# Optimization experiments

Hardware: AMD Instinct MI355X
Metric: run time of the kernel (lower is better)

Reference implementation:

```python
import jax, jax.numpy as jnp
import numpy as np

L = 4            # n_layers
D_MODEL = 768
D_STATE = 16
D_CONV = 4
EXPAND = 2
D_INNER = EXPAND * D_MODEL      # 1536
DT_RANK = (D_MODEL + 15) // 16  # 48
B = 2
T = 2048
LN_EPS = 1e-5


def setup_inputs() -> dict:
    key = jax.random.key(0)
    ks = jax.random.split(key, 12)
    s = 0.02
    x = jax.random.normal(ks[0], (B, T, D_MODEL), dtype=jnp.float32)
    in_proj_w = jax.random.normal(ks[1], (L, 2 * D_INNER, D_MODEL), dtype=jnp.float32) * s
    conv_w = jax.random.normal(ks[2], (L, D_INNER, D_CONV), dtype=jnp.float32) * s
    conv_b = jnp.zeros((L, D_INNER), dtype=jnp.float32)
    x_proj_w = jax.random.normal(ks[3], (L, DT_RANK + 2 * D_STATE, D_INNER), dtype=jnp.float32) * s
    dt_proj_w = jax.random.normal(ks[4], (L, D_INNER, DT_RANK), dtype=jnp.float32) * s
    dt_proj_b = jax.random.normal(ks[5], (L, D_INNER), dtype=jnp.float32) * 0.1
    # Standard S4D-real init: A = -[1..d_state], stored as log
    A_log = jnp.log(jnp.broadcast_to(
        jnp.arange(1, D_STATE + 1, dtype=jnp.float32), (L, D_INNER, D_STATE)))
    D_param = jnp.ones((L, D_INNER), dtype=jnp.float32)
    out_proj_w = jax.random.normal(ks[6], (L, D_MODEL, D_INNER), dtype=jnp.float32) * s
    ln_g = jnp.ones((L, D_MODEL), dtype=jnp.float32)
    ln_b = jnp.zeros((L, D_MODEL), dtype=jnp.float32)
    return {"x": x, "in_proj_w": in_proj_w, "conv_w": conv_w, "conv_b": conv_b,
            "x_proj_w": x_proj_w, "dt_proj_w": dt_proj_w, "dt_proj_b": dt_proj_b,
            "A_log": A_log, "D_param": D_param, "out_proj_w": out_proj_w,
            "ln_g": ln_g, "ln_b": ln_b}


def _layernorm(x, g, b):
    mu = jnp.mean(x, axis=-1, keepdims=True)
    var = jnp.mean(jnp.square(x - mu), axis=-1, keepdims=True)
    return (x - mu) * jax.lax.rsqrt(var + LN_EPS) * g + b


def _mamba_layer(x, inw, convw, convb, xpw, dtw, dtb, A_log, Dp, outw):
    # x: [B,T,d_model]
    Tn = x.shape[1]
    xz = jnp.einsum('btd,ed->bte', x, inw)          # [B,T,2*d_inner]
    xin, z = jnp.split(xz, 2, axis=-1)              # each [B,T,d_inner]
    # causal depthwise conv1d over time (kernel d_conv)
    xp = jnp.pad(xin, ((0, 0), (D_CONV - 1, 0), (0, 0)))
    xc = convb
    for k in range(D_CONV):
        xc = xc + xp[:, k:k + Tn, :] * convw[:, k]
    xc = jax.nn.silu(xc)                            # [B,T,d_inner]
    dbl = jnp.einsum('bti,ei->bte', xc, xpw)        # [B,T,dt_rank+2*d_state]
    dt, Bs, Cs = jnp.split(dbl, [DT_RANK, DT_RANK + D_STATE], axis=-1)
    dt = jax.nn.softplus(jnp.einsum('btr,dr->btd', dt, dtw) + dtb)  # [B,T,d_inner]
    A = -jnp.exp(A_log)                             # [d_inner,d_state]
    dA = jnp.exp(jnp.einsum('btd,dn->btdn', dt, A))  # discretized A
    dBu = (dt * xc)[..., None] * Bs[:, :, None, :]   # [B,T,d_inner,d_state]

    def step(h, inp):
        dA_t, dBu_t, C_t = inp                      # [B,d,n],[B,d,n],[B,n]
        h = dA_t * h + dBu_t
        y = jnp.einsum('bdn,bn->bd', h, C_t)
        return h, y

    h0 = jnp.zeros((x.shape[0], D_INNER, D_STATE), x.dtype)
    _, ys = jax.lax.scan(step, h0,
                         (jnp.swapaxes(dA, 0, 1), jnp.swapaxes(dBu, 0, 1),
                          jnp.swapaxes(Cs, 0, 1)))
    y = jnp.swapaxes(ys, 0, 1) + xc * Dp            # skip connection D*u
    y = y * jax.nn.silu(z)                          # gate
    return jnp.einsum('bti,ei->bte', y, outw)       # [B,T,d_model]


def reference(x, in_proj_w, conv_w, conv_b, x_proj_w, dt_proj_w, dt_proj_b,
              A_log, D_param, out_proj_w, ln_g, ln_b):
    for l in range(L):
        residual = x
        h = _mamba_layer(x, in_proj_w[l], conv_w[l], conv_b[l], x_proj_w[l],
                         dt_proj_w[l], dt_proj_b[l], A_log[l], D_param[l],
                         out_proj_w[l])
        h = _layernorm(h, ln_g[l], ln_b[l])
        x = h + residual                            # dropout=0 -> identity
    return x
```

## Files before the change

kernel.cpp:

```cpp
#include <hip/hip_runtime.h>

#define T_LEN 2048
#define DM    768
#define DI    1536
#define DS    16
#define BB    2
#define NROWS (BB * T_LEN)
#define NCH   64
#define CLEN  32
#define NSEG  8
#define SEGC  8

#define OFF_DTB 0
#define OFF_A   6144
#define OFF_DP  104448
#define OFF_CW  110592
#define OFF_CB  135168
#define OFF_LG  141312
#define OFF_LB  144384
#define PRM_TOT 147456

typedef __attribute__((ext_vector_type(8))) short bh8;
typedef __attribute__((ext_vector_type(4))) float f32x4;

typedef const __attribute__((address_space(1))) void as1_void;
typedef __attribute__((address_space(3))) void as3_void;

__device__ __forceinline__ void glds16(const void* g, void* l) {
    __builtin_amdgcn_global_load_lds((as1_void*)g, (as3_void*)l, 16, 0, 0);
}

__device__ __forceinline__ float bf2f(unsigned short u) {
    return __uint_as_float(((unsigned)u) << 16);
}
__device__ __forceinline__ unsigned short f2bf(float f) {
    unsigned u = __float_as_uint(f);
    u += 0x7FFFu + ((u >> 16) & 1u);
    return (unsigned short)(u >> 16);
}

__device__ __forceinline__ void ld8(const void* p, long e0, int bf, float* v) {
    if (bf) {
        bh8 u = *(const bh8*)((const unsigned short*)p + e0);
#pragma unroll
        for (int j = 0; j < 8; ++j) v[j] = bf2f((unsigned short)u[j]);
    } else {
        const f32x4* q = (const f32x4*)((const float*)p + e0);
        f32x4 a = q[0], b = q[1];
#pragma unroll
        for (int j = 0; j < 4; ++j) { v[j] = a[j]; v[4 + j] = b[j]; }
    }
}

__device__ __forceinline__ void cp8(unsigned short* dst, long de0,
                                    const void* src, long se0, int bf) {
    if (bf) {
        *(bh8*)&dst[de0] = *(const bh8*)((const unsigned short*)src + se0);
    } else {
        const f32x4* q = (const f32x4*)((const float*)src + se0);
        f32x4 a = q[0], b = q[1];
        bh8 o;
#pragma unroll
        for (int j = 0; j < 4; ++j) { o[j] = (short)f2bf(a[j]); o[4 + j] = (short)f2bf(b[j]); }
        *(bh8*)&dst[de0] = o;
    }
}

__global__ void k_sniff(const unsigned short* __restrict__ x, int* __restrict__ flag) {
    __shared__ int cnt[4];
    int tid = threadIdx.x;
    int local = 0;
#pragma unroll
    for (int j = 0; j < 4; ++j) {
        unsigned short u = x[tid * 4 + j];
        int e = (u >> 7) & 0xFF;
        if (e >= 100 && e <= 140) local++;
    }
    for (int off = 32; off; off >>= 1) local += __shfl_down(local, off, 64);
    if ((tid & 63) == 0) cnt[tid >> 6] = local;
    __syncthreads();
    if (tid == 0) {
        int tot = cnt[0] + cnt[1] + cnt[2] + cnt[3];
        *flag = (tot >= 900) ? 1 : 0;
    }
}

__global__ void k_prep(const void* in_x, const void* in_inw, const void* in_ow,
                       const void* in_xpw, const void* in_dtw,
                       const void* dtb, const void* alog, const void* dpar,
                       const void* cw, const void* cb, const void* lg, const void* lb,
                       unsigned short* __restrict__ xbf, float* __restrict__ xf,
                       unsigned short* __restrict__ Win, unsigned short* __restrict__ Wout,
                       unsigned short* __restrict__ Wxp, unsigned short* __restrict__ Wdt,
                       float* __restrict__ prm, float* __restrict__ dblz,
                       const int* __restrict__ flag) {
    const long G0 = 393216L;
    const long G1 = G0 + 1179648L;
    const long G2 = G1 + 589824L;
    const long G3 = G2 + 98304L;
    const long G4 = G3 + 49152L;
    const long G5 = G4 + 18432L;
    const long G6 = G5 + 65536L;
    int bf = *flag;
    long g = (long)blockIdx.x * 256 + threadIdx.x;
    if (g >= G6) return;
    if (g < G0) {
        long e0 = g * 8;
        float v[8];
        ld8(in_x, e0, bf, v);
        bh8 o;
#pragma unroll
        for (int j = 0; j < 8; ++j) o[j] = (short)f2bf(v[j]);
        *(bh8*)&xbf[e0] = o;
        f32x4 a, b;
#pragma unroll
        for (int j = 0; j < 4; ++j) { a[j] = v[j]; b[j] = v[4 + j]; }
        ((f32x4*)&xf[e0])[0] = a;
        ((f32x4*)&xf[e0])[1] = b;
    } else if (g < G1) {
        long e0 = (g - G0) * 8;
        cp8(Win, e0, in_inw, e0, bf);
    } else if (g < G2) {
        long e0 = (g - G1) * 8;
        cp8(Wout, e0, in_ow, e0, bf);
    } else if (g < G3) {
        long e0 = (g - G2) * 8;
        int c = (int)(e0 % 1536);
        long rl = e0 / 1536;
        int r = (int)(rl % 128);
        int l = (int)(rl / 128);
        if (r < 80) cp8(Wxp, e0, in_xpw, ((long)l * 80 + r) * 1536 + c, bf);
        else        *(bh8*)&Wxp[e0] = (bh8)(short)0;
    } else if (g < G4) {
        long e0 = (g - G3) * 8;
        int c = (int)(e0 & 63);
        long rl = e0 >> 6;
        int d = (int)(rl % 1536);
        int l = (int)(rl / 1536);
        if (c < 48) cp8(Wdt, e0, in_dtw, ((long)l * 1536 + d) * 48 + c, bf);
        else        *(bh8*)&Wdt[e0] = (bh8)(short)0;
    } else if (g < G5) {
        long e0 = (g - G4) * 8;
        float v[8];
        if (e0 < OFF_A)        ld8(dtb,  e0 - OFF_DTB, bf, v);
        else if (e0 < OFF_DP) {
            ld8(alog, e0 - OFF_A, bf, v);
#pragma unroll
            for (int j = 0; j < 8; ++j) v[j] = -__expf(v[j]);
        }
        else if (e0 < OFF_CW)  ld8(dpar, e0 - OFF_DP, bf, v);
        else if (e0 < OFF_CB)  ld8(cw,   e0 - OFF_CW, bf, v);
        else if (e0 < OFF_LG)  ld8(cb,   e0 - OFF_CB, bf, v);
        else if (e0 < OFF_LB)  ld8(lg,   e0 - OFF_LG, bf, v);
        else                   ld8(lb,   e0 - OFF_LB, bf, v);
        f32x4 a, b;
#pragma unroll
        for (int j = 0; j < 4; ++j) { a[j] = v[j]; b[j] = v[4 + j]; }
        ((f32x4*)&prm[e0])[0] = a;
        ((f32x4*)&prm[e0])[1] = b;
    } else {
        long e0 = (g - G5) * 8;
        f32x4 z = {0.f, 0.f, 0.f, 0.f};
        ((f32x4*)&dblz[e0])[0] = z;
        ((f32x4*)&dblz[e0])[1] = z;
    }
}

__global__ __launch_bounds__(256) void k_gemm128(const unsigned short* __restrict__ A,
                                                 const unsigned short* __restrict__ B,
                                                 unsigned short* __restrict__ C,
                                                 int M, int N, int K) {
    __shared__ __align__(16) unsigned short As[128 * 32];
    __shared__ __align__(16) unsigned short Bs[128 * 32];
    const int tid = threadIdx.x;
    const int lane = tid & 63, wid = tid >> 6;
    const int wm = wid >> 1, wn = wid & 1;
    const int id = blockIdx.y * 24 + blockIdx.x;
    const int xcd = id & 7, loc = id >> 3;
    const int bx = (xcd & 1) * 12 + loc % 12;
    const int by = (xcd >> 1) * 8 + loc / 12;
    const long arow0 = (long)by * 128;
    const long bcol0 = (long)bx * 128;
    const int r16 = lane >> 2;
    const int c8  = (lane & 3) * 8;
    f32x4 acc[4][4] = {};

    for (int k0 = 0; k0 < K; k0 += 32) {
#pragma unroll
        for (int j = 0; j < 2; ++j) {
            int chunk = wid + j * 4;
            int row = chunk * 16 + r16;
            glds16(&A[(arow0 + row) * K + k0 + c8], &As[chunk * 512]);
            glds16(&B[(bcol0 + row) * K + k0 + c8], &Bs[chunk * 512]);
        }
        __syncthreads();
        const int row = lane & 15, q8 = (lane >> 4) * 8;
        bh8 af[4], bfr[4];
#pragma unroll
        for (int i = 0; i < 4; ++i) af[i] = *(const bh8*)&As[(wm * 64 + i * 16 + row) * 32 + q8];
#pragma unroll
        for (int i = 0; i < 4; ++i) bfr[i] = *(const bh8*)&Bs[(wn * 64 + i * 16 + row) * 32 + q8];
#pragma unroll
        for (int i = 0; i < 4; ++i)
#pragma unroll
            for (int j = 0; j < 4; ++j)
                acc[i][j] = __builtin_amdgcn_mfma_f32_16x16x32_bf16(af[i], bfr[j], acc[i][j], 0, 0, 0);
        __syncthreads();
    }
    const int crow = (lane >> 4) * 4, ccol = lane & 15;
#pragma unroll
    for (int i = 0; i < 4; ++i)
#pragma unroll
        for (int j = 0; j < 4; ++j)
#pragma unroll
            for (int r = 0; r < 4; ++r) {
                long gr = arow0 + wm * 64 + i * 16 + crow + r;
                long gc = bcol0 + wn * 64 + j * 16 + ccol;
                C[gr * N + gc] = f2bf(acc[i][j][r]);
            }
}

__global__ __launch_bounds__(256) void k_xproj(const unsigned short* __restrict__ xz,
                                               const unsigned short* __restrict__ B,
                                               const float* __restrict__ cw,
                                               const float* __restrict__ cb,
                                               float* __restrict__ C) {
    __shared__ __align__(16) unsigned short As[64 * 32];
    __shared__ __align__(16) unsigned short Bs[64 * 32];
    const int tid = threadIdx.x;
    const int lane = tid & 63, w = tid >> 6;
    const int wm = w >> 1, wn = w & 1;
    const long arow0 = (long)blockIdx.y * 64;
    const long bcol0 = (long)blockIdx.x * 64;
    const int kbase = blockIdx.z * 384;
    const int r4 = lane >> 2;
    const int c8 = (lane & 3) * 8;
    const int t_o = tid >> 2;
    const int dl  = (tid & 3) * 8;
    const int sp  = (int)((arow0 + t_o) & (T_LEN - 1));
    f32x4 acc[2][2] = {};

    for (int kk = 0; kk < 384; kk += 32) {
        const int k0 = kbase + kk;
        glds16(&B[(bcol0 + w * 16 + r4) * DI + k0 + c8], &Bs[w * 512]);
        const int dg = k0 + dl;
        float xv[4][8];
#pragma unroll
        for (int rr = 0; rr < 4; ++rr) {
            if (sp - 3 + rr >= 0) {
                bh8 u = *(const bh8*)&xz[(arow0 + t_o - 3 + rr) * 3072 + dg];
#pragma unroll
                for (int q = 0; q < 8; ++q) xv[rr][q] = bf2f((unsigned short)u[q]);
            } else {
#pragma unroll
                for (int q = 0; q < 8; ++q) xv[rr][q] = 0.f;
            }
        }
        bh8 o;
#pragma unroll
        for (int q = 0; q < 8; ++q) {
            const f32x4 w4 = *(const f32x4*)&cw[(dg + q) * 4];
            float a = cb[dg + q] + w4[0] * xv[0][q] + w4[1] * xv[1][q]
                                 + w4[2] * xv[2][q] + w4[3] * xv[3][q];
            a = a / (1.f + __expf(-a));
            o[q] = (short)f2bf(a);
        }
        *(bh8*)&As[t_o * 32 + dl] = o;
        __syncthreads();
        const int row2 = lane & 15, q8 = (lane >> 4) * 8;
        bh8 af[2], bfr[2];
#pragma unroll
        for (int i = 0; i < 2; ++i) af[i] = *(const bh8*)&As[(wm * 32 + i * 16 + row2) * 32 + q8];
#pragma unroll
        for (int i = 0; i < 2; ++i) bfr[i] = *(const bh8*)&Bs[(wn * 32 + i * 16 + row2) * 32 + q8];
#pragma unroll
        for (int i = 0; i < 2; ++i)
#pragma unroll
            for (int j = 0; j < 2; ++j)
                acc[i][j] = __builtin_amdgcn_mfma_f32_16x16x32_bf16(af[i], bfr[j], acc[i][j], 0, 0, 0);
        __syncthreads();
    }
    const int crow = (lane >> 4) * 4, ccol = lane & 15;
#pragma unroll
    for (int i = 0; i < 2; ++i)
#pragma unroll
        for (int j = 0; j < 2; ++j)
#pragma unroll
            for (int r = 0; r < 4; ++r) {
                long gr = arow0 + wm * 32 + i * 16 + crow + r;
                long gc = bcol0 + wn * 32 + j * 16 + ccol;
                atomicAdd(&C[gr * 128 + gc], acc[i][j][r]);
            }
}

__global__ __launch_bounds__(256) void k_dtproj(const float* __restrict__ Dbl,
                                                const unsigned short* __restrict__ Wdt,
                                                const float* __restrict__ bias,
                                                unsigned short* __restrict__ Dt) {
    __shared__ __align__(16) unsigned short As[2 * 64 * 32];
    __shared__ __align__(16) unsigned short Bs[2 * 64 * 32];
    const int tid = threadIdx.x;
    const int lane = tid & 63, wid = tid >> 6;
    const int wm = wid >> 1, wn = wid & 1;
    const long arow0 = (long)blockIdx.y * 64;
    const long bcol0 = (long)blockIdx.x * 64;

    {
        int r = tid >> 2;
        int cs = (tid & 3) * 16;
        unsigned short tmp[16];
#pragma unroll
        for (int q = 0; q < 4; ++q) {
            int col0 = cs + q * 4;
            if (col0 < 48) {
                f32x4 v = *(const f32x4*)&Dbl[(arow0 + r) * 128 + col0];
#pragma unroll
                for (int j = 0; j < 4; ++j) tmp[q * 4 + j] = f2bf(v[j]);
            } else {
#pragma unroll
                for (int j = 0; j < 4; ++j) tmp[q * 4 + j] = 0;
            }
        }
        int p = cs >> 5;
        int cp = cs & 31;
        *(bh8*)&As[p * 2048 + r * 32 + cp]     = *(bh8*)&tmp[0];
        *(bh8*)&As[p * 2048 + r * 32 + cp + 8] = *(bh8*)&tmp[8];
    }
#pragma unroll
    for (int j = 0; j < 2; ++j) {
        int chunk = tid + j * 256;
        int p = chunk >> 8;
        int rem = chunk & 255;
        int row = rem >> 2;
        int c4 = rem & 3;
        glds16(&Wdt[(bcol0 + row) * 64 + p * 32 + c4 * 8], &Bs[chunk * 8]);
    }
    __syncthreads();

    const int row2 = lane & 15, q8 = (lane >> 4) * 8;
    f32x4 acc[2][2] = {};
#pragma unroll
    for (int p = 0; p < 2; ++p) {
        bh8 af[2], bfr[2];
#pragma unroll
        for (int i = 0; i < 2; ++i) af[i] = *(const bh8*)&As[p * 2048 + (wm * 32 + i * 16 + row2) * 32 + q8];
#pragma unroll
        for (int i = 0; i < 2; ++i) bfr[i] = *(const bh8*)&Bs[p * 2048 + (wn * 32 + i * 16 + row2) * 32 + q8];
#pragma unroll
        for (int i = 0; i < 2; ++i)
#pragma unroll
            for (int j = 0; j < 2; ++j)
                acc[i][j] = __builtin_amdgcn_mfma_f32_16x16x32_bf16(af[i], bfr[j], acc[i][j], 0, 0, 0);
    }
    const int crow = (lane >> 4) * 4, ccol = lane & 15;
#pragma unroll
    for (int i = 0; i < 2; ++i)
#pragma unroll
        for (int j = 0; j < 2; ++j)
#pragma unroll
            for (int r = 0; r < 4; ++r) {
                long gr = arow0 + wm * 32 + i * 16 + crow + r;
                long gc = bcol0 + wn * 32 + j * 16 + ccol;
                float v = acc[i][j][r] + bias[gc];
                v = (v > 20.f) ? v : log1pf(__expf(v));
                Dt[gr * DI + gc] = f2bf(v);
            }
}

__global__ __launch_bounds__(256) void k_outproj(const unsigned short* __restrict__ A,
                                                 const unsigned short* __restrict__ B,
                                                 float* __restrict__ C) {
    __shared__ __align__(16) unsigned short As[64 * 32];
    __shared__ __align__(16) unsigned short Bs[64 * 32];
    const int tid = threadIdx.x;
    const int lane = tid & 63, wid = tid >> 6;
    const int wm = wid >> 1, wn = wid & 1;
    const int id = blockIdx.y * 12 + blockIdx.x;
    const int xcd = id & 7, loc = id >> 3;
    const int bx = (xcd & 1) * 6 + loc % 6;
    const int by = (xcd >> 1) * 16 + loc / 6;
    const long arow0 = (long)by * 64;
    const long bcol0 = (long)bx * 64;
    const int r16 = lane >> 2;
    const int c8  = (lane & 3) * 8;
    f32x4 acc[2][2] = {};

    for (int k0 = 0; k0 < DI; k0 += 32) {
        int row = wid * 16 + r16;
        glds16(&A[(arow0 + row) * DI + k0 + c8], &As[wid * 512]);
        glds16(&B[(bcol0 + row) * DI + k0 + c8], &Bs[wid * 512]);
        __syncthreads();
        const int row2 = lane & 15, q8 = (lane >> 4) * 8;
        bh8 af[2], bfr[2];
#pragma unroll
        for (int i = 0; i < 2; ++i) af[i] = *(const bh8*)&As[(wm * 32 + i * 16 + row2) * 32 + q8];
#pragma unroll
        for (int i = 0; i < 2; ++i) bfr[i] = *(const bh8*)&Bs[(wn * 32 + i * 16 + row2) * 32 + q8];
#pragma unroll
        for (int i = 0; i < 2; ++i)
#pragma unroll
            for (int j = 0; j < 2; ++j)
                acc[i][j] = __builtin_amdgcn_mfma_f32_16x16x32_bf16(af[i], bfr[j], acc[i][j], 0, 0, 0);
        __syncthreads();
    }
    const int crow = (lane >> 4) * 4, ccol = lane & 15;
#pragma unroll
    for (int i = 0; i < 2; ++i)
#pragma unroll
        for (int j = 0; j < 2; ++j)
#pragma unroll
            for (int r = 0; r < 4; ++r) {
                long gr = arow0 + wm * 32 + i * 16 + crow + r;
                long gc = bcol0 + wn * 32 + j * 16 + ccol;
                C[gr * DM + gc] = acc[i][j][r];
            }
}

__global__ __launch_bounds__(256) void k_scan1(const unsigned short* __restrict__ dt,
                                               const unsigned short* __restrict__ xz,
                                               const float* __restrict__ dbl,
                                               const float* __restrict__ An,
                                               const float* __restrict__ cw,
                                               const float* __restrict__ cb,
                                               float* __restrict__ hch,
                                               float* __restrict__ sdtb) {
    __shared__ __align__(16) float Bsh[CLEN * 16];
    const int tid = threadIdx.x;
    const int lane = tid & 63, w = tid >> 6;
    const int db = blockIdx.x % 6;
    const int c  = (blockIdx.x / 6) % NCH;
    const int b  = blockIdx.x / (6 * NCH);
    const int d  = db * 256 + tid;
    const int t0 = c * CLEN;
    const long rowb = (long)b * T_LEN + t0;
    if (w < 2) {
        int t = w * 16 + (lane >> 2);
        int nq = lane & 3;
        glds16(&dbl[(rowb + t) * 128 + 48 + nq * 4], &Bsh[w * 256]);
    }
    float h[DS], An_r[DS];
    const f32x4* Ap = (const f32x4*)(An + (long)d * DS);
#pragma unroll
    for (int q = 0; q < 4; ++q) {
        f32x4 a4 = Ap[q];
#pragma unroll
        for (int j = 0; j < 4; ++j) { An_r[q * 4 + j] = a4[j]; h[q * 4 + j] = 0.f; }
    }
    const f32x4 w4 = *(const f32x4*)&cw[d * 4];
    const float cbv = cb[d];
    float x1, x2, x3;
    if (c == 0) { x1 = x2 = x3 = 0.f; }
    else {
        x1 = bf2f(xz[(rowb - 1) * 3072 + d]);
        x2 = bf2f(xz[(rowb - 2) * 3072 + d]);
        x3 = bf2f(xz[(rowb - 3) * 3072 + d]);
    }
    __syncthreads();
    float sdt = 0.f;
#pragma unroll 4
    for (int s = 0; s < CLEN; ++s) {
        long bt = rowb + s;
        float xt = bf2f(xz[bt * 3072 + d]);
        float a = cbv + w4[0] * x3 + w4[1] * x2 + w4[2] * x1 + w4[3] * xt;
        float xcv = a / (1.f + __expf(-a));
        x3 = x2; x2 = x1; x1 = xt;
        float dtv = bf2f(dt[bt * DI + d]);
        const f32x4* bp = (const f32x4*)&Bsh[s * 16];
        float du = dtv * xcv;
        sdt += dtv;
#pragma unroll
        for (int q = 0; q < 4; ++q) {
            f32x4 b4 = bp[q];
#pragma unroll
            for (int j = 0; j < 4; ++j) {
                int n = q * 4 + j;
                h[n] = __expf(An_r[n] * dtv) * h[n] + du * b4[j];
            }
        }
    }
    long o = (((long)b * NCH + c) * DI + d) * DS;
    f32x4* hp = (f32x4*)(hch + o);
#pragma unroll
    for (int q = 0; q < 4; ++q) {
        f32x4 h4;
#pragma unroll
        for (int j = 0; j < 4; ++j) h4[j] = h[q * 4 + j];
        hp[q] = h4;
    }
    sdtb[((long)b * NCH + c) * DI + d] = sdt;
}

__global__ __launch_bounds__(256) void k_scan2a(float* __restrict__ hbuf,
                                                const float* __restrict__ sdtb,
                                                const float* __restrict__ An,
                                                float* __restrict__ cum,
                                                float* __restrict__ Gseg,
                                                float* __restrict__ Sseg) {
    long gid = (long)blockIdx.x * 256 + threadIdx.x;
    int n = (int)(gid & 15);
    long t = gid >> 4;
    int d  = (int)(t % DI);
    int sg = (int)((t / DI) & (NSEG - 1));
    int b  = (int)(t / (DI * NSEG));
    float an = An[(long)d * DS + n];
    float h = 0.f, cs = 0.f;
    for (int i = 0; i < SEGC; ++i) {
        int c = sg * SEGC + i;
        long rowi = ((long)b * NCH + c) * DI + d;
        long idx = rowi * DS + n;
        float sdt = sdtb[rowi];
        float g = hbuf[idx];
        hbuf[idx] = h;
        if (n == 0) cum[rowi] = cs;
        h = __expf(an * sdt) * h + g;
        cs += sdt;
    }
    long gi = (((long)b * NSEG + sg) * DI + d) * DS + n;
    Gseg[gi] = h;
    if (n == 0) Sseg[((long)b * NSEG + sg) * DI + d] = cs;
}

__global__ __launch_bounds__(256) void k_scan3(const unsigned short* __restrict__ dt,
                                               const unsigned short* __restrict__ xz,
                                               const float* __restrict__ dbl,
                                               const float* __restrict__ An,
                                               const float* __restrict__ cw,
                                               const float* __restrict__ cb,
                                               const float* __restrict__ Dp,
                                               const float* __restrict__ hpref,
                                               const float* __restrict__ cum,
                                               const float* __restrict__ Gseg,
                                               const float* __restrict__ Sseg,
                                               unsigned short* __restrict__ ybf) {
    __shared__ __align__(16) float Bsh[CLEN * 16];
    __shared__ __align__(16) float Csh[CLEN * 16];
    const int tid = threadIdx.x;
    const int lane = tid & 63, w = tid >> 6;
    const int db = blockIdx.x % 6;
    const int c  = (blockIdx.x / 6) % NCH;
    const int b  = blockIdx.x / (6 * NCH);
    const int d  = db * 256 + tid;
    const int t0 = c * CLEN;
    const int sg = c / SEGC;
    const long rowb = (long)b * T_LEN + t0;
    if (w < 2) {
        int t = w * 16 + (lane >> 2);
        glds16(&dbl[(rowb + t) * 128 + 48 + (lane & 3) * 4], &Bsh[w * 256]);
    } else {
        int t = (w - 2) * 16 + (lane >> 2);
        glds16(&dbl[(rowb + t) * 128 + 64 + (lane & 3) * 4], &Csh[(w - 2) * 256]);
    }
    float h[DS], An_r[DS];
    long rowi = ((long)b * NCH + c) * DI + d;
    long o = rowi * DS;
    const float cs = cum[rowi];
    const f32x4* Ap = (const f32x4*)(An + (long)d * DS);
#pragma unroll
    for (int q = 0; q < 4; ++q) {
        f32x4 a4 = Ap[q];
#pragma unroll
        for (int j = 0; j < 4; ++j) An_r[q * 4 + j] = a4[j];
    }
    float Hn[DS];
#pragma unroll
    for (int n = 0; n < DS; ++n) Hn[n] = 0.f;
    for (int s2 = 0; s2 < sg; ++s2) {
        long gi = (((long)b * NSEG + s2) * DI + d) * DS;
        float S = Sseg[((long)b * NSEG + s2) * DI + d];
        const f32x4* Gp = (const f32x4*)(Gseg + gi);
#pragma unroll
        for (int q = 0; q < 4; ++q) {
            f32x4 g4 = Gp[q];
#pragma unroll
            for (int j = 0; j < 4; ++j) {
                int n = q * 4 + j;
                Hn[n] = __expf(An_r[n] * S) * Hn[n] + g4[j];
            }
        }
    }
    const f32x4* Pp = (const f32x4*)(hpref + o);
#pragma unroll
    for (int q = 0; q < 4; ++q) {
        f32x4 p4 = Pp[q];
#pragma unroll
        for (int j = 0; j < 4; ++j) {
            int n = q * 4 + j;
            h[n] = __expf(An_r[n] * cs) * Hn[n] + p4[j];
        }
    }
    const float dcoef = Dp[d];
    const f32x4 w4 = *(const f32x4*)&cw[d * 4];
    const float cbv = cb[d];
    float x1, x2, x3;
    if (c == 0) { x1 = x2 = x3 = 0.f; }
    else {
        x1 = bf2f(xz[(rowb - 1) * 3072 + d]);
        x2 = bf2f(xz[(rowb - 2) * 3072 + d]);
        x3 = bf2f(xz[(rowb - 3) * 3072 + d]);
    }
    __syncthreads();
#pragma unroll 4
    for (int s = 0; s < CLEN; ++s) {
        long bt = rowb + s;
        float xt = bf2f(xz[bt * 3072 + d]);
        float a = cbv + w4[0] * x3 + w4[1] * x2 + w4[2] * x1 + w4[3] * xt;
        float xcv = a / (1.f + __expf(-a));
        x3 = x2; x2 = x1; x1 = xt;
        float dtv = bf2f(dt[bt * DI + d]);
        const f32x4* bp = (const f32x4*)&Bsh[s * 16];
        const f32x4* cp = (const f32x4*)&Csh[s * 16];
        float du = dtv * xcv;
        float yp[4] = {xcv * dcoef, 0.f, 0.f, 0.f};
#pragma unroll
        for (int q = 0; q < 4; ++q) {
            f32x4 b4 = bp[q], c4 = cp[q];
#pragma unroll
            for (int j = 0; j < 4; ++j) {
                int n = q * 4 + j;
                h[n] = __expf(An_r[n] * dtv) * h[n] + du * b4[j];
                yp[j] += h[n] * c4[j];
            }
        }
        float y = (yp[0] + yp[1]) + (yp[2] + yp[3]);
        float zv = bf2f(xz[bt * 3072 + DI + d]);
        y *= zv / (1.f + __expf(-zv));
        ybf[bt * DI + d] = f2bf(y);
    }
}

__global__ __launch_bounds__(256) void k_ln(const float* __restrict__ prj,
                                            float* __restrict__ x,
                                            unsigned short* __restrict__ xbf,
                                            const float* __restrict__ lg,
                                            const float* __restrict__ lb,
                                            void* __restrict__ dout,
                                            float* __restrict__ dblz,
                                            int is_last, const int* __restrict__ flag) {
    __shared__ float red[8];
    const int row = blockIdx.x;
    const int tid = threadIdx.x;
    float v[3];
    float s = 0.f, s2 = 0.f;
#pragma unroll
    for (int j = 0; j < 3; ++j) {
        v[j] = prj[(long)row * DM + tid + j * 256];
        s += v[j];
        s2 += v[j] * v[j];
    }
    for (int off = 32; off; off >>= 1) {
        s  += __shfl_down(s, off, 64);
        s2 += __shfl_down(s2, off, 64);
    }
    if ((tid & 63) == 0) { red[tid >> 6] = s; red[4 + (tid >> 6)] = s2; }
    __syncthreads();
    float S  = red[0] + red[1] + red[2] + red[3];
    float S2 = red[4] + red[5] + red[6] + red[7];
    float mu = S * (1.f / DM);
    float var = S2 * (1.f / DM) - mu * mu;
    float rs = rsqrtf(var + 1e-5f);
    int bf = *flag;
#pragma unroll
    for (int j = 0; j < 3; ++j) {
        int e = tid + j * 256;
        long idx = (long)row * DM + e;
        float out = (v[j] - mu) * rs * lg[e] + lb[e] + x[idx];
        x[idx] = out;
        xbf[idx] = f2bf(out);
        if (is_last) {
            if (bf) ((unsigned short*)dout)[idx] = f2bf(out);
            else    ((float*)dout)[idx] = out;
        }
    }
    long gid = (long)row * 256 + tid;
    if (gid < 524288) dblz[gid] = 0.f;
}

extern "C" void kernel_launch(void* const* d_in, const int* in_sizes, int n_in,
                              void* d_out, int out_size, void* d_ws, size_t ws_size,
                              hipStream_t stream) {
    char* ws = (char*)d_ws;
    const size_t O_FLAG = 0;
    const size_t O_WIN  = 256;
    const size_t O_WXP  = O_WIN  + 18874368;
    const size_t O_WDT  = O_WXP  + 1572864;
    const size_t O_WOUT = O_WDT  + 786432;
    const size_t O_PRM  = O_WOUT + 9437184;
    const size_t O_XBF  = O_PRM  + 589824;
    const size_t O_XF   = O_XBF  + 6291456;
    const size_t O_XZ   = O_XF   + 12582912;
    const size_t O_DBL  = O_XZ   + 25165824;
    const size_t O_DT   = O_DBL  + 2097152;
    const size_t O_HCH  = O_DT   + 12582912;
    const size_t O_SDT  = O_HCH  + 12582912;
    const size_t O_CUM  = O_SDT  + 786432;
    const size_t O_GSEG = O_CUM  + 786432;
    const size_t O_SSEG = O_GSEG + 1572864;
    const size_t O_YBF  = O_SSEG + 98304;

    int* flag = (int*)(ws + O_FLAG);
    unsigned short* Win  = (unsigned short*)(ws + O_WIN);
    unsigned short* Wxp  = (unsigned short*)(ws + O_WXP);
    unsigned short* Wdt  = (unsigned short*)(ws + O_WDT);
    unsigned short* Wout = (unsigned short*)(ws + O_WOUT);
    float* prm = (float*)(ws + O_PRM);
    unsigned short* Xbf = (unsigned short*)(ws + O_XBF);
    float* Xf  = (float*)(ws + O_XF);
    unsigned short* Xz = (unsigned short*)(ws + O_XZ);
    float* Dbl = (float*)(ws + O_DBL);
    unsigned short* Dt = (unsigned short*)(ws + O_DT);
    float* Hch = (float*)(ws + O_HCH);
    float* Sdt = (float*)(ws + O_SDT);
    float* Cum = (float*)(ws + O_CUM);
    float* Gsg = (float*)(ws + O_GSEG);
    float* Ssg = (float*)(ws + O_SSEG);
    unsigned short* Ybf = (unsigned short*)(ws + O_YBF);
    float* Prj = (float*)(ws + O_XZ);

    k_sniff<<<1, 256, 0, stream>>>((const unsigned short*)d_in[0], flag);
    k_prep<<<9352, 256, 0, stream>>>(d_in[0], d_in[1], d_in[9], d_in[4], d_in[5],
                                     d_in[6], d_in[7], d_in[8], d_in[2], d_in[3],
                                     d_in[10], d_in[11],
                                     Xbf, Xf, Win, Wout, Wxp, Wdt, prm, Dbl, flag);

    for (int l = 0; l < 4; ++l) {
        const unsigned short* winL  = Win  + (size_t)l * 3072 * 768;
        const unsigned short* wxpL  = Wxp  + (size_t)l * 128 * 1536;
        const unsigned short* wdtL  = Wdt  + (size_t)l * 1536 * 64;
        const unsigned short* woutL = Wout + (size_t)l * 768 * 1536;
        const float* cwL  = prm + OFF_CW  + (size_t)l * DI * 4;
        const float* cbL  = prm + OFF_CB  + (size_t)l * DI;
        const float* dtbL = prm + OFF_DTB + (size_t)l * DI;
        const float* anL  = prm + OFF_A   + (size_t)l * DI * DS;
        const float* dpL  = prm + OFF_DP  + (size_t)l * DI;
        const float* lgL  = prm + OFF_LG  + (size_t)l * DM;
        const float* lbL  = prm + OFF_LB  + (size_t)l * DM;

        k_gemm128<<<dim3(24, 32), 256, 0, stream>>>(Xbf, winL, Xz, NROWS, 2 * DI, DM);
        k_xproj<<<dim3(2, 64, 4), 256, 0, stream>>>(Xz, wxpL, cwL, cbL, Dbl);
        k_dtproj<<<dim3(24, 64), 256, 0, stream>>>(Dbl, wdtL, dtbL, Dt);
        k_scan1<<<BB * NCH * 6, 256, 0, stream>>>(Dt, Xz, Dbl, anL, cwL, cbL, Hch, Sdt);
        k_scan2a<<<1536, 256, 0, stream>>>(Hch, Sdt, anL, Cum, Gsg, Ssg);
        k_scan3<<<BB * NCH * 6, 256, 0, stream>>>(Dt, Xz, Dbl, anL, cwL, cbL, dpL,
                                                  Hch, Cum, Gsg, Ssg, Ybf);
        k_outproj<<<dim3(12, 64), 256, 0, stream>>>(Ybf, woutL, Prj);
        k_ln<<<4096, 256, 0, stream>>>(Prj, Xf, Xbf, lgL, lbL, d_out, Dbl,
                                       (l == 3) ? 1 : 0, flag);
    }
}
```

Baseline: 935.1 us.

## Materialize causal conv+SiLU once in a dedicated kernel instead of recomputing

```diff
diff --git a/kernel.cpp b/kernel.cpp
--- a/kernel.cpp
+++ b/kernel.cpp
@@ -220,52 +220,55 @@
             }
 }
 
-__global__ __launch_bounds__(256) void k_xproj(const unsigned short* __restrict__ xz,
+__global__ __launch_bounds__(256) void k_conv(const unsigned short* __restrict__ xz,
+                                              const float* __restrict__ cw,
+                                              const float* __restrict__ cb,
+                                              unsigned short* __restrict__ xcbf) {
+    __shared__ float tile[131 * 64];
+    const int tid = threadIdx.x;
+    const int d0 = blockIdx.x * 64;
+    const long t0 = (long)blockIdx.y * 128;
+    const bool seqstart = ((int)t0 & (T_LEN - 1)) == 0;
+    for (int j = tid; j < 131 * 64; j += 256) {
+        int row = j >> 6, col = j & 63;
+        float v = 0.f;
+        if (!(seqstart && row < 3)) v = bf2f(xz[(t0 - 3 + row) * 3072 + d0 + col]);
+        tile[j] = v;
+    }
+    __syncthreads();
+    const int d = tid & 63, tl0 = tid >> 6;
+    const int dg = d0 + d;
+    const float w0 = cw[dg * 4 + 0], w1 = cw[dg * 4 + 1];
+    const float w2 = cw[dg * 4 + 2], w3 = cw[dg * 4 + 3];
+    const float bias = cb[dg];
+    for (int tt = tl0; tt < 128; tt += 4) {
+        float acc = bias + w0 * tile[tt * 64 + d] + w1 * tile[(tt + 1) * 64 + d]
+                         + w2 * tile[(tt + 2) * 64 + d] + w3 * tile[(tt + 3) * 64 + d];
+        float s = acc / (1.f + __expf(-acc));
+        xcbf[(t0 + tt) * DI + dg] = f2bf(s);
+    }
+}
+
+__global__ __launch_bounds__(256) void k_xproj(const unsigned short* __restrict__ A,
                                                const unsigned short* __restrict__ B,
-                                               const float* __restrict__ cw,
-                                               const float* __restrict__ cb,
                                                float* __restrict__ C) {
     __shared__ __align__(16) unsigned short As[64 * 32];
     __shared__ __align__(16) unsigned short Bs[64 * 32];
     const int tid = threadIdx.x;
-    const int lane = tid & 63, w = tid >> 6;
-    const int wm = w >> 1, wn = w & 1;
+    const int lane = tid & 63, wid = tid >> 6;
+    const int wm = wid >> 1, wn = wid & 1;
     const long arow0 = (long)blockIdx.y * 64;
     const long bcol0 = (long)blockIdx.x * 64;
     const int kbase = blockIdx.z * 384;
-    const int r4 = lane >> 2;
-    const int c8 = (lane & 3) * 8;
-    const int t_o = tid >> 2;
-    const int dl  = (tid & 3) * 8;
-    const int sp  = (int)((arow0 + t_o) & (T_LEN - 1));
+    const int r16 = lane >> 2;
+    const int c8  = (lane & 3) * 8;
     f32x4 acc[2][2] = {};
 
     for (int kk = 0; kk < 384; kk += 32) {
-        const int k0 = kbase + kk;
-        glds16(&B[(bcol0 + w * 16 + r4) * DI + k0 + c8], &Bs[w * 512]);
-        const int dg = k0 + dl;
-        float xv[4][8];
-#pragma unroll
-        for (int rr = 0; rr < 4; ++rr) {
-            if (sp - 3 + rr >= 0) {
-                bh8 u = *(const bh8*)&xz[(arow0 + t_o - 3 + rr) * 3072 + dg];
-#pragma unroll
-                for (int q = 0; q < 8; ++q) xv[rr][q] = bf2f((unsigned short)u[q]);
-            } else {
-#pragma unroll
-                for (int q = 0; q < 8; ++q) xv[rr][q] = 0.f;
-            }
-        }
-        bh8 o;
-#pragma unroll
-        for (int q = 0; q < 8; ++q) {
-            const f32x4 w4 = *(const f32x4*)&cw[(dg + q) * 4];
-            float a = cb[dg + q] + w4[0] * xv[0][q] + w4[1] * xv[1][q]
-                                 + w4[2] * xv[2][q] + w4[3] * xv[3][q];
-            a = a / (1.f + __expf(-a));
-            o[q] = (short)f2bf(a);
-        }
-        *(bh8*)&As[t_o * 32 + dl] = o;
+        int k0 = kbase + kk;
+        int row = wid * 16 + r16;
+        glds16(&A[(arow0 + row) * DI + k0 + c8], &As[wid * 512]);
+        glds16(&B[(bcol0 + row) * DI + k0 + c8], &Bs[wid * 512]);
         __syncthreads();
         const int row2 = lane & 15, q8 = (lane >> 4) * 8;
         bh8 af[2], bfr[2];
@@ -417,11 +420,9 @@
 }
 
 __global__ __launch_bounds__(256) void k_scan1(const unsigned short* __restrict__ dt,
-                                               const unsigned short* __restrict__ xz,
+                                               const unsigned short* __restrict__ xcbf,
                                                const float* __restrict__ dbl,
                                                const float* __restrict__ An,
-                                               const float* __restrict__ cw,
-                                               const float* __restrict__ cb,
                                                float* __restrict__ hch,
                                                float* __restrict__ sdtb) {
     __shared__ __align__(16) float Bsh[CLEN * 16];
@@ -435,8 +436,7 @@
     const long rowb = (long)b * T_LEN + t0;
     if (w < 2) {
         int t = w * 16 + (lane >> 2);
-        int nq = lane & 3;
-        glds16(&dbl[(rowb + t) * 128 + 48 + nq * 4], &Bsh[w * 256]);
+        glds16(&dbl[(rowb + t) * 128 + 48 + (lane & 3) * 4], &Bsh[w * 256]);
     }
     float h[DS], An_r[DS];
     const f32x4* Ap = (const f32x4*)(An + (long)d * DS);
@@ -445,25 +445,13 @@
         f32x4 a4 = Ap[q];
 #pragma unroll
         for (int j = 0; j < 4; ++j) { An_r[q * 4 + j] = a4[j]; h[q * 4 + j] = 0.f; }
-    }
-    const f32x4 w4 = *(const f32x4*)&cw[d * 4];
-    const float cbv = cb[d];
-    float x1, x2, x3;
-    if (c == 0) { x1 = x2 = x3 = 0.f; }
-    else {
-        x1 = bf2f(xz[(rowb - 1) * 3072 + d]);
-        x2 = bf2f(xz[(rowb - 2) * 3072 + d]);
-        x3 = bf2f(xz[(rowb - 3) * 3072 + d]);
     }
     __syncthreads();
     float sdt = 0.f;
 #pragma unroll 4
     for (int s = 0; s < CLEN; ++s) {
         long bt = rowb + s;
-        float xt = bf2f(xz[bt * 3072 + d]);
-        float a = cbv + w4[0] * x3 + w4[1] * x2 + w4[2] * x1 + w4[3] * xt;
-        float xcv = a / (1.f + __expf(-a));
-        x3 = x2; x2 = x1; x1 = xt;
+        float xcv = bf2f(xcbf[bt * DI + d]);
         float dtv = bf2f(dt[bt * DI + d]);
         const f32x4* bp = (const f32x4*)&Bsh[s * 16];
         float du = dtv * xcv;
@@ -521,11 +509,10 @@
 }
 
 __global__ __launch_bounds__(256) void k_scan3(const unsigned short* __restrict__ dt,
+                                               const unsigned short* __restrict__ xcbf,
                                                const unsigned short* __restrict__ xz,
                                                const float* __restrict__ dbl,
                                                const float* __restrict__ An,
-                                               const float* __restrict__ cw,
-                                               const float* __restrict__ cb,
                                                const float* __restrict__ Dp,
                                                const float* __restrict__ hpref,
                                                const float* __restrict__ cum,
@@ -589,23 +576,11 @@
         }
     }
     const float dcoef = Dp[d];
-    const f32x4 w4 = *(const f32x4*)&cw[d * 4];
-    const float cbv = cb[d];
-    float x1, x2, x3;
-    if (c == 0) { x1 = x2 = x3 = 0.f; }
-    else {
-        x1 = bf2f(xz[(rowb - 1) * 3072 + d]);
-        x2 = bf2f(xz[(rowb - 2) * 3072 + d]);
-        x3 = bf2f(xz[(rowb - 3) * 3072 + d]);
-    }
     __syncthreads();
 #pragma unroll 4
     for (int s = 0; s < CLEN; ++s) {
         long bt = rowb + s;
-        float xt = bf2f(xz[bt * 3072 + d]);
-        float a = cbv + w4[0] * x3 + w4[1] * x2 + w4[2] * x1 + w4[3] * xt;
-        float xcv = a / (1.f + __expf(-a));
-        x3 = x2; x2 = x1; x1 = xt;
+        float xcv = bf2f(xcbf[bt * DI + d]);
         float dtv = bf2f(dt[bt * DI + d]);
         const f32x4* bp = (const f32x4*)&Bsh[s * 16];
         const f32x4* cp = (const f32x4*)&Csh[s * 16];
@@ -688,7 +663,8 @@
     const size_t O_XBF  = O_PRM  + 589824;
     const size_t O_XF   = O_XBF  + 6291456;
     const size_t O_XZ   = O_XF   + 12582912;
-    const size_t O_DBL  = O_XZ   + 25165824;
+    const size_t O_XCBF = O_XZ   + 25165824;
+    const size_t O_DBL  = O_XCBF + 12582912;
     const size_t O_DT   = O_DBL  + 2097152;
     const size_t O_HCH  = O_DT   + 12582912;
     const size_t O_SDT  = O_HCH  + 12582912;
@@ -706,6 +682,7 @@
     unsigned short* Xbf = (unsigned short*)(ws + O_XBF);
     float* Xf  = (float*)(ws + O_XF);
     unsigned short* Xz = (unsigned short*)(ws + O_XZ);
+    unsigned short* Xcbf = (unsigned short*)(ws + O_XCBF);
     float* Dbl = (float*)(ws + O_DBL);
     unsigned short* Dt = (unsigned short*)(ws + O_DT);
     float* Hch = (float*)(ws + O_HCH);
@@ -736,11 +713,12 @@
         const float* lbL  = prm + OFF_LB  + (size_t)l * DM;
 
         k_gemm128<<<dim3(24, 32), 256, 0, stream>>>(Xbf, winL, Xz, NROWS, 2 * DI, DM);
-        k_xproj<<<dim3(2, 64, 4), 256, 0, stream>>>(Xz, wxpL, cwL, cbL, Dbl);
+        k_conv<<<dim3(24, 32), 256, 0, stream>>>(Xz, cwL, cbL, Xcbf);
+        k_xproj<<<dim3(2, 64, 4), 256, 0, stream>>>(Xcbf, wxpL, Dbl);
         k_dtproj<<<dim3(24, 64), 256, 0, stream>>>(Dbl, wdtL, dtbL, Dt);
-        k_scan1<<<BB * NCH * 6, 256, 0, stream>>>(Dt, Xz, Dbl, anL, cwL, cbL, Hch, Sdt);
+        k_scan1<<<BB * NCH * 6, 256, 0, stream>>>(Dt, Xcbf, Dbl, anL, Hch, Sdt);
         k_scan2a<<<1536, 256, 0, stream>>>(Hch, Sdt, anL, Cum, Gsg, Ssg);
-        k_scan3<<<BB * NCH * 6, 256, 0, stream>>>(Dt, Xz, Dbl, anL, cwL, cbL, dpL,
+        k_scan3<<<BB * NCH * 6, 256, 0, stream>>>(Dt, Xcbf, Xz, Dbl, anL, dpL,
                                                   Hch, Cum, Gsg, Ssg, Ybf);
         k_outproj<<<dim3(12, 64), 256, 0, stream>>>(Ybf, woutL, Prj);
         k_ln<<<4096, 256, 0, stream>>>(Prj, Xf, Xbf, lgL, lbL, d_out, Dbl,
```

After: 864.4 us. 1.08x faster.
